# Kernel tuning notes

Measured on AMD Instinct MI355X. Metric: run time of the kernel, lower is better.

Reference implementation:

```python
import jax, jax.numpy as jnp
import numpy as np

D_MODEL = 3072
NUM_EXPERTS = 8
TOP_K = 2
BATCH, SEQ = 4, 4096


def setup_inputs() -> dict:
    key = jax.random.key(0)
    kx, kw, kb = jax.random.split(key, 3)
    x = jax.random.normal(kx, (BATCH, SEQ, D_MODEL), dtype=jnp.float32)
    W = jax.random.normal(kw, (NUM_EXPERTS, D_MODEL), dtype=jnp.float32) * (1.0 / np.sqrt(D_MODEL))
    b = jax.random.normal(kb, (NUM_EXPERTS,), dtype=jnp.float32) * 0.02
    return {"x": x, "W": W, "b": b}


def reference(x, W, b):
    # Linear gate: [B, S, D] x [E, D]^T -> [B, S, E]
    logits = jnp.einsum("bsd,ed->bse", x, W) + b
    gate_scores = jax.nn.softmax(logits, axis=-1)
    # top-k over experts
    topk_values, topk_indices = jax.lax.top_k(gate_scores, TOP_K)
    # renormalize the selected scores with a second softmax
    topk_values = jax.nn.softmax(topk_values, axis=-1)
    return (topk_values, topk_indices)
```

## Files before the change

### kernel.cpp

```cpp
#include <hip/hip_runtime.h>


#define NTOK   16384
#define DMODEL 3072
#define NEXP   8
#define NDB    16
#define DCH    (DMODEL / NDB)
#define DS     32
#define NSUB   (DCH / DS)
#define TPB    256

__global__ __launch_bounds__(TPB) void gate_logits_kernel(
    const float* __restrict__ x, const float* __restrict__ W,
    float* __restrict__ logits) {
  __shared__ float xt[TPB][DS + 1];

  const int tid = threadIdx.x;
  const int tokBase = blockIdx.x * TPB;
  const int dBase = blockIdx.y * DCH;

  float acc[NEXP];
#pragma unroll
  for (int e = 0; e < NEXP; ++e) acc[e] = 0.f;

  for (int s = 0; s < NSUB; ++s) {
    const int dc = dBase + s * DS;
#pragma unroll
    for (int i = 0; i < 8; ++i) {
      const int f = i * TPB + tid;
      const int tok = f >> 3;
      const int d4 = (f & 7) << 2;
      const float4 v =
          *(const float4*)&x[(size_t)(tokBase + tok) * DMODEL + dc + d4];
      xt[tok][d4 + 0] = v.x;
      xt[tok][d4 + 1] = v.y;
      xt[tok][d4 + 2] = v.z;
      xt[tok][d4 + 3] = v.w;
    }
    __syncthreads();

#pragma unroll
    for (int j = 0; j < DS; ++j) {
      const float xv = xt[tid][j];
#pragma unroll
      for (int e = 0; e < NEXP; ++e) {
        acc[e] = fmaf(xv, W[e * DMODEL + dc + j], acc[e]);
      }
    }
    __syncthreads();
  }

#pragma unroll
  for (int e = 0; e < NEXP; ++e) {
    atomicAdd(&logits[(size_t)(tokBase + tid) * NEXP + e], acc[e]);
  }
}

__global__ __launch_bounds__(256) void gate_topk_kernel(
    const float* __restrict__ logits, const float* __restrict__ bias,
    float* __restrict__ out) {
  const int t = blockIdx.x * blockDim.x + threadIdx.x;
  if (t >= NTOK) return;

  float l[NEXP];
#pragma unroll
  for (int e = 0; e < NEXP; ++e) l[e] = logits[(size_t)t * NEXP + e] + bias[e];

  float m = l[0];
#pragma unroll
  for (int e = 1; e < NEXP; ++e) m = fmaxf(m, l[e]);

  float p[NEXP];
  float ssum = 0.f;
#pragma unroll
  for (int e = 0; e < NEXP; ++e) {
    p[e] = expf(l[e] - m);
    ssum += p[e];
  }
  const float inv = 1.f / ssum;
#pragma unroll
  for (int e = 0; e < NEXP; ++e) p[e] *= inv;

  int i1 = 0;
  float v1 = p[0];
#pragma unroll
  for (int e = 1; e < NEXP; ++e) {
    if (p[e] > v1) { v1 = p[e]; i1 = e; }
  }
  int i2 = -1;
  float v2 = -1.f;
#pragma unroll
  for (int e = 0; e < NEXP; ++e) {
    if (e == i1) continue;
    if (p[e] > v2) { v2 = p[e]; i2 = e; }
  }

  const float e2 = expf(v2 - v1);
  const float r = 1.f / (1.f + e2);

  out[(size_t)t * 2 + 0] = r;
  out[(size_t)t * 2 + 1] = e2 * r;
  out[2 * NTOK + (size_t)t * 2 + 0] = (float)i1;
  out[2 * NTOK + (size_t)t * 2 + 1] = (float)i2;
}

extern "C" void kernel_launch(void* const* d_in, const int* in_sizes, int n_in,
                              void* d_out, int out_size, void* d_ws,
                              size_t ws_size, hipStream_t stream) {
  const float* x = (const float*)d_in[0];
  const float* W = (const float*)d_in[1];
  const float* b = (const float*)d_in[2];
  float* out = (float*)d_out;
  float* logits = (float*)d_ws;

  hipMemsetAsync(d_ws, 0, (size_t)NTOK * NEXP * sizeof(float), stream);

  dim3 grid1(NTOK / TPB, NDB);
  gate_logits_kernel<<<grid1, TPB, 0, stream>>>(x, W, logits);

  gate_topk_kernel<<<NTOK / 256, 256, 0, stream>>>(logits, b, out);
}
```

Measured before the change: 329.6 us.

## Double-buffer x tiles via direct global-to-LDS loads with XOR swizzle

```diff
diff --git a/kernel.cpp b/kernel.cpp
--- a/kernel.cpp
+++ b/kernel.cpp
@@ -1,53 +1,79 @@
 #include <hip/hip_runtime.h>
+#include <stdint.h>
 
 
 #define NTOK   16384
 #define DMODEL 3072
 #define NEXP   8
-#define NDB    16
+#define NDB    8
 #define DCH    (DMODEL / NDB)
 #define DS     32
-#define NSUB   (DCH / DS)
+#define NST    (DCH / DS)
 #define TPB    256
+
+typedef __attribute__((address_space(1))) const void gvoid;
+typedef __attribute__((address_space(3))) void lvoid;
 
 __global__ __launch_bounds__(TPB) void gate_logits_kernel(
     const float* __restrict__ x, const float* __restrict__ W,
     float* __restrict__ logits) {
-  __shared__ float xt[TPB][DS + 1];
+  __shared__ float4 sbuf[2][2048];
 
   const int tid = threadIdx.x;
+  const int wave = tid >> 6;
+  const int lane = tid & 63;
   const int tokBase = blockIdx.x * TPB;
   const int dBase = blockIdx.y * DCH;
+
+  auto issue_stage = [&](int s, int b) {
+    const int d0 = dBase + s * DS;
+#pragma unroll
+    for (int k = 0; k < 8; ++k) {
+      const int c = wave * 8 + k;
+      const int g = c * 64 + lane;
+      const int tok = g >> 3;
+      const int slot = g & 7;
+      const int d4 = slot ^ (tok & 7);
+      const float* gp =
+          x + (size_t)(tokBase + tok) * DMODEL + d0 + d4 * 4;
+      __builtin_amdgcn_global_load_lds((gvoid*)gp, (lvoid*)&sbuf[b][c * 64],
+                                       16, 0, 0);
+    }
+  };
 
   float acc[NEXP];
 #pragma unroll
   for (int e = 0; e < NEXP; ++e) acc[e] = 0.f;
 
-  for (int s = 0; s < NSUB; ++s) {
-    const int dc = dBase + s * DS;
+  issue_stage(0, 0);
+  issue_stage(1, 1);
+
+  for (int s = 0; s < NST; ++s) {
+    if (s < NST - 1) {
+      asm volatile("s_waitcnt vmcnt(8)\n\ts_barrier" ::: "memory");
+    } else {
+      asm volatile("s_waitcnt vmcnt(0)\n\ts_barrier" ::: "memory");
+    }
+
+    const int b = s & 1;
+    const int d0 = dBase + s * DS;
+    const float4* row = &sbuf[b][tid * 8];
 #pragma unroll
-    for (int i = 0; i < 8; ++i) {
-      const int f = i * TPB + tid;
-      const int tok = f >> 3;
-      const int d4 = (f & 7) << 2;
-      const float4 v =
-          *(const float4*)&x[(size_t)(tokBase + tok) * DMODEL + dc + d4];
-      xt[tok][d4 + 0] = v.x;
-      xt[tok][d4 + 1] = v.y;
-      xt[tok][d4 + 2] = v.z;
-      xt[tok][d4 + 3] = v.w;
-    }
-    __syncthreads();
-
-#pragma unroll
-    for (int j = 0; j < DS; ++j) {
-      const float xv = xt[tid][j];
+    for (int q = 0; q < 8; ++q) {
+      const float4 xv = row[q ^ (tid & 7)];
+      const int dw = d0 + q * 4;
 #pragma unroll
       for (int e = 0; e < NEXP; ++e) {
-        acc[e] = fmaf(xv, W[e * DMODEL + dc + j], acc[e]);
+        const float* wr = &W[e * DMODEL + dw];
+        acc[e] = fmaf(xv.x, wr[0],
+                 fmaf(xv.y, wr[1],
+                 fmaf(xv.z, wr[2],
+                 fmaf(xv.w, wr[3], acc[e]))));
       }
     }
-    __syncthreads();
+
+    asm volatile("s_waitcnt lgkmcnt(0)\n\ts_barrier" ::: "memory");
+    if (s + 2 < NST) issue_stage(s + 2, b);
   }
 
 #pragma unroll
@@ -56,10 +82,10 @@
   }
 }
 
-__global__ __launch_bounds__(256) void gate_topk_kernel(
+__global__ __launch_bounds__(64) void gate_topk_kernel(
     const float* __restrict__ logits, const float* __restrict__ bias,
     float* __restrict__ out) {
-  const int t = blockIdx.x * blockDim.x + threadIdx.x;
+  const int t = blockIdx.x * 64 + threadIdx.x;
   if (t >= NTOK) return;
 
   float l[NEXP];
@@ -118,5 +144,5 @@
   dim3 grid1(NTOK / TPB, NDB);
   gate_logits_kernel<<<grid1, TPB, 0, stream>>>(x, W, logits);
 
-  gate_topk_kernel<<<NTOK / 256, 256, 0, stream>>>(logits, b, out);
+  gate_topk_kernel<<<NTOK / 64, 64, 0, stream>>>(logits, b, out);
 }
```

Result: slower. 338.2 us (+2.6%).
